# Kernel optimization log

Hardware: AMD Instinct MI355X
Metric: run time of the kernel (lower is better)

Reference implementation:

```python
import jax, jax.numpy as jnp
import numpy as np

N = 100_000      # nodes
E = 1_600_000    # edges (avg degree 16)
C_IN = 32
C_OUT = 32


def setup_inputs() -> dict:
    key = jax.random.key(0)
    ks = jax.random.split(key, 8)
    x = jax.random.normal(ks[0], (N, C_IN), jnp.float32)
    edge_index = jax.random.randint(ks[1], (2, E), 0, N)
    edge_weight = jax.random.uniform(ks[2], (E,), jnp.float32)
    h = jax.random.normal(ks[3], (N, C_OUT), jnp.float32)
    s_in = 1.0 / np.sqrt(C_IN)
    s_out = 1.0 / np.sqrt(C_OUT)
    # 6 ChebConvs (gates z, r, h-tilde; each has an x-conv and an h-conv), K=2
    Wx = jax.random.normal(ks[4], (3, 2, C_IN, C_OUT), jnp.float32) * s_in
    bx = jnp.zeros((3, C_OUT), jnp.float32)
    Wh = jax.random.normal(ks[5], (3, 2, C_OUT, C_OUT), jnp.float32) * s_out
    bh = jnp.zeros((3, C_OUT), jnp.float32)
    Wl = jax.random.normal(ks[6], (C_OUT, 1), jnp.float32) * s_out
    bl = jnp.zeros((1,), jnp.float32)
    return dict(x=x, edge_index=edge_index, edge_weight=edge_weight, h=h,
                Wx=Wx, bx=bx, Wh=Wh, bh=bh, Wl=Wl, bl=bl)


def _cheb(v, W, b, coef, src, dst, n):
    # ChebConv, K=2, sym norm, lambda_max=2:
    #   T0 = v ; T1 = Lhat @ v, Lhat = -D^{-1/2} A D^{-1/2} (zero diagonal)
    t1 = jax.ops.segment_sum(coef[:, None] * v[src], dst, num_segments=n)
    return v @ W[0] + t1 @ W[1] + b


def reference(x, edge_index, edge_weight, h, Wx, bx, Wh, bh, Wl, bl):
    n = x.shape[0]
    src, dst = edge_index[0], edge_index[1]
    deg = jax.ops.segment_sum(edge_weight, src, num_segments=n)
    safe = jnp.where(deg > 0, deg, 1.0)
    dis = jnp.where(deg > 0, jax.lax.rsqrt(safe), 0.0)
    coef = -(dis[src] * edge_weight * dis[dst])  # scaled-Laplacian edge coeffs

    def gate(g, v_x, v_h):
        return (_cheb(v_x, Wx[g], bx[g], coef, src, dst, n)
                + _cheb(v_h, Wh[g], bh[g], coef, src, dst, n))

    z = jax.nn.sigmoid(gate(0, x, h))          # update gate
    r = jax.nn.sigmoid(gate(1, x, h))          # reset gate
    h_tilde = jnp.tanh(gate(2, x, h * r))      # candidate state
    h_new = z * h + (1.0 - z) * h_tilde
    out = jax.nn.softplus(jax.nn.relu(h_new) @ Wl + bl)  # [N, 1]
    return (out, h_new)
```

## Files before the change

kernel.cpp:

```cpp
#include <hip/hip_runtime.h>
#include <math.h>

#define NN 100000
#define NE 1600000
#define C  32
#define CAP 48

#define BSH    8
#define BNODES 256
#define NB     392
#define BCAP   4608
#define EPB    4096

#define WQ_SCALE 32767.0f
#define INV_WQ   (1.0f/32767.0f)
#define DEG_FIX  4194304.0f
#define INV_DEG_FIX (1.0f/4194304.0f)

typedef __attribute__((ext_vector_type(8))) short short8;
typedef __attribute__((ext_vector_type(4))) float floatx4;

__device__ __forceinline__ unsigned rn_bf16(float f) {
    unsigned b = __float_as_uint(f);
    return (b + 0x7fffu + ((b >> 16) & 1u)) >> 16;
}

__device__ __forceinline__ float sigm(float a) { return 1.f / (1.f + expf(-a)); }

__device__ __forceinline__ unsigned enc_edge(int s, float w) {
    int wq = (int)(w * WQ_SCALE + 0.5f);
    wq = wq > 32767 ? 32767 : wq;
    return ((unsigned)s << 15) | (unsigned)wq;
}

__device__ __forceinline__ short8 pack_hi8(uint4 a, uint4 b) {
    short8 v;
    v[0] = (short)(a.x >> 16); v[1] = (short)(a.y >> 16);
    v[2] = (short)(a.z >> 16); v[3] = (short)(a.w >> 16);
    v[4] = (short)(b.x >> 16); v[5] = (short)(b.y >> 16);
    v[6] = (short)(b.z >> 16); v[7] = (short)(b.w >> 16);
    return v;
}
__device__ __forceinline__ short8 pack_lo8(uint4 a, uint4 b) {
    short8 v;
    v[0] = (short)(a.x & 0xffffu); v[1] = (short)(a.y & 0xffffu);
    v[2] = (short)(a.z & 0xffffu); v[3] = (short)(a.w & 0xffffu);
    v[4] = (short)(b.x & 0xffffu); v[5] = (short)(b.y & 0xffffu);
    v[6] = (short)(b.z & 0xffffu); v[7] = (short)(b.w & 0xffffu);
    return v;
}

__global__ __launch_bounds__(256) void bin_pass(const int* __restrict__ ei,
                                                const float* __restrict__ w,
                                                int* __restrict__ gbin_d,
                                                int* __restrict__ gbin_s,
                                                uint2* __restrict__ drec,
                                                unsigned* __restrict__ srec) {
    __shared__ int hd[NB], hs[NB], bd[NB], bs[NB];
    int tid = threadIdx.x;
    for (int i = tid; i < NB; i += 256) { hd[i] = 0; hs[i] = 0; }
    __syncthreads();
    int e0 = blockIdx.x * EPB;
    for (int i = tid; i < EPB; i += 256) {
        int e = e0 + i;
        if (e < NE) {
            atomicAdd(&hs[ei[e] >> BSH], 1);
            atomicAdd(&hd[ei[NE + e] >> BSH], 1);
        }
    }
    __syncthreads();
    for (int i = tid; i < NB; i += 256) {
        bd[i] = hd[i] ? atomicAdd(&gbin_d[i], hd[i]) : 0;
        bs[i] = hs[i] ? atomicAdd(&gbin_s[i], hs[i]) : 0;
    }
    __syncthreads();
    for (int i = tid; i < NB; i += 256) { hd[i] = 0; hs[i] = 0; }
    __syncthreads();
    for (int i = tid; i < EPB; i += 256) {
        int e = e0 + i;
        if (e < NE) {
            int s = ei[e], d = ei[NE + e];
            float we = w[e];
            int dbin = d >> BSH;
            int off = bd[dbin] + atomicAdd(&hd[dbin], 1);
            if (off < BCAP)
                drec[(size_t)dbin * BCAP + off] =
                    make_uint2(((unsigned)s << BSH) | (unsigned)(d & (BNODES - 1)),
                               __float_as_uint(we));
            int sbin = s >> BSH;
            int offs = bs[sbin] + atomicAdd(&hs[sbin], 1);
            if (offs < BCAP)
                srec[(size_t)sbin * BCAP + offs] =
                    ((unsigned)(s & (BNODES - 1)) << 22) | (unsigned)(we * DEG_FIX);
        }
    }
}

__global__ __launch_bounds__(256) void bin_build(const uint2* __restrict__ drec,
                                                 const unsigned* __restrict__ srec,
                                                 const int* __restrict__ gbin_d,
                                                 const int* __restrict__ gbin_s,
                                                 unsigned* __restrict__ buckets,
                                                 int* __restrict__ cursor,
                                                 float* __restrict__ dis) {
    __shared__ __align__(16) unsigned lbuck[BNODES * CAP];
    __shared__ int lcur[BNODES];
    __shared__ int ldeg[BNODES];
    int b = blockIdx.x, tid = threadIdx.x;
    if (tid < BNODES) { lcur[tid] = 0; ldeg[tid] = 0; }
    __syncthreads();
    int cnt_d = min(gbin_d[b], BCAP);
    int cnt_s = min(gbin_s[b], BCAP);
    for (int i = tid; i < cnt_d; i += 256) {
        uint2 r = drec[(size_t)b * BCAP + i];
        int d8 = r.x & (BNODES - 1);
        int s  = (int)(r.x >> BSH);
        int pos = atomicAdd(&lcur[d8], 1);
        if (pos < CAP) lbuck[d8 * CAP + pos] = enc_edge(s, __uint_as_float(r.y));
    }
    for (int i = tid; i < cnt_s; i += 256) {
        unsigned r = srec[(size_t)b * BCAP + i];
        atomicAdd(&ldeg[r >> 22], (int)(r & 0x3FFFFFu));
    }
    __syncthreads();
    uint4* gb = (uint4*)(buckets + (size_t)b * BNODES * CAP);
    const uint4* lb = (const uint4*)lbuck;
    for (int i = tid; i < BNODES * CAP / 4; i += 256) gb[i] = lb[i];
    int n = b * BNODES + tid;
    if (tid < BNODES && n < NN) {
        cursor[n] = lcur[tid];
        int di = ldeg[tid];
        dis[n] = di > 0 ? rsqrtf((float)di * INV_DEG_FIX) : 0.f;
    }
}

__global__ __launch_bounds__(256) void build_xh(const float* __restrict__ x,
                                                const float* __restrict__ h,
                                                const float* __restrict__ dis,
                                                unsigned* __restrict__ xh2,
                                                unsigned* __restrict__ xraw2) {
    int t = blockIdx.x * 256 + threadIdx.x;
    if (t >= NN * C) return;
    float d = dis[t >> 5];
    float xv = x[t], hv = h[t];
    xh2[t]   = (rn_bf16(xv * d) << 16) | rn_bf16(hv * d);
    xraw2[t] = (rn_bf16(xv) << 16) | rn_bf16(hv);
}

__global__ __launch_bounds__(256) void agg_xh(const unsigned* __restrict__ buckets,
                                              const int* __restrict__ cursor,
                                              const float* __restrict__ dis,
                                              const unsigned* __restrict__ xh2,
                                              unsigned* __restrict__ agg2) {
    int tid = threadIdx.x;
    int nl = tid >> 5, j = tid & 31;
    int n = blockIdx.x * 8 + nl;
    if (n >= NN) return;
    int cnt = min(cursor[n], CAP);
    float ax0 = 0.f, ax1 = 0.f, ax2 = 0.f, ax3 = 0.f;
    float ah0 = 0.f, ah1 = 0.f, ah2 = 0.f, ah3 = 0.f;
    for (int base = 0; base < cnt; base += 32) {
        int idx = base + j;
        int sv = 0; float cv = 0.f;
        if (idx < cnt) {
            unsigned u = buckets[(size_t)n * CAP + idx];
            sv = (int)(u >> 15);
            cv = (float)(u & 32767u) * INV_WQ;
        }
        int mm = min(32, cnt - base);
        int i2 = 0;
        for (; i2 + 4 <= mm; i2 += 4) {
            int s0 = __shfl(sv, i2 + 0, 32); float c0 = __shfl(cv, i2 + 0, 32);
            int s1 = __shfl(sv, i2 + 1, 32); float c1 = __shfl(cv, i2 + 1, 32);
            int s2 = __shfl(sv, i2 + 2, 32); float c2 = __shfl(cv, i2 + 2, 32);
            int s3 = __shfl(sv, i2 + 3, 32); float c3 = __shfl(cv, i2 + 3, 32);
            unsigned u0 = xh2[(size_t)s0 * C + j];
            unsigned u1 = xh2[(size_t)s1 * C + j];
            unsigned u2 = xh2[(size_t)s2 * C + j];
            unsigned u3 = xh2[(size_t)s3 * C + j];
            ax0 = fmaf(c0, __uint_as_float(u0 & 0xffff0000u), ax0);
            ah0 = fmaf(c0, __uint_as_float(u0 << 16), ah0);
            ax1 = fmaf(c1, __uint_as_float(u1 & 0xffff0000u), ax1);
            ah1 = fmaf(c1, __uint_as_float(u1 << 16), ah1);
            ax2 = fmaf(c2, __uint_as_float(u2 & 0xffff0000u), ax2);
            ah2 = fmaf(c2, __uint_as_float(u2 << 16), ah2);
            ax3 = fmaf(c3, __uint_as_float(u3 & 0xffff0000u), ax3);
            ah3 = fmaf(c3, __uint_as_float(u3 << 16), ah3);
        }
        for (; i2 < mm; ++i2) {
            int s = __shfl(sv, i2, 32); float cf = __shfl(cv, i2, 32);
            unsigned u = xh2[(size_t)s * C + j];
            ax0 = fmaf(cf, __uint_as_float(u & 0xffff0000u), ax0);
            ah0 = fmaf(cf, __uint_as_float(u << 16), ah0);
        }
    }
    float disn = -dis[n];
    float ax = disn * ((ax0 + ax1) + (ax2 + ax3));
    float ah = disn * ((ah0 + ah1) + (ah2 + ah3));
    agg2[(size_t)n * C + j] = (rn_bf16(ax) << 16) | rn_bf16(ah);
}

__global__ __launch_bounds__(256) void gate_mfma(const unsigned* __restrict__ xraw2,
                                                 const unsigned* __restrict__ agg2,
                                                 const float* __restrict__ dis,
                                                 const float* __restrict__ Wx,
                                                 const float* __restrict__ Wh,
                                                 const float* __restrict__ bx,
                                                 const float* __restrict__ bh,
                                                 unsigned* __restrict__ hrz2,
                                                 unsigned short* __restrict__ hr16,
                                                 float* __restrict__ pout) {
    __shared__ __align__(16) unsigned short Bl[20][64][8];
    int tid = threadIdx.x;
    for (int i = tid; i < 20 * 64; i += 256) {
        int f = i >> 6, l = i & 63;
        int t, c;
        if (f < 16) { t = f >> 2; c = f & 3; }
        else        { t = 4 + ((f - 16) >> 1); c = (f - 16) & 1; }
        int g = t >> 1;
        int j = ((t & 1) << 4) + (l & 15);
        int kb = (l >> 4) << 3;
        const float* srcp = (c < 2 ? Wx : Wh) + g * 2048 + (c & 1) * 1024 + j;
        unsigned pk[4];
#pragma unroll
        for (int q = 0; q < 4; ++q) {
            unsigned lo = rn_bf16(srcp[(kb + 2 * q) * 32]);
            unsigned hi = rn_bf16(srcp[(kb + 2 * q + 1) * 32]);
            pk[q] = (hi << 16) | lo;
        }
        *(uint4*)(&Bl[f][l][0]) = make_uint4(pk[0], pk[1], pk[2], pk[3]);
    }

    int lane = tid & 63, wave = tid >> 6;
    int j0 = lane & 15, quad = lane >> 4;
    int tbase = blockIdx.x * 64 + wave * 16;
    int na = tbase + j0;
    short8 A0 = {0,0,0,0,0,0,0,0}, A1 = A0, A2 = A0, A3 = A0;
    if (na < NN) {
        const uint4* px = (const uint4*)(xraw2 + (size_t)na * C + quad * 8);
        uint4 xa = px[0], xb = px[1];
        A0 = pack_hi8(xa, xb);
        A2 = pack_lo8(xa, xb);
        const uint4* pg = (const uint4*)(agg2 + (size_t)na * C + quad * 8);
        uint4 ga = pg[0], gb = pg[1];
        A1 = pack_hi8(ga, gb);
        A3 = pack_lo8(ga, gb);
    }
    __syncthreads();

#define B8(f) (*(const short8*)(&Bl[f][lane][0]))
    floatx4 az0 = {0.f,0.f,0.f,0.f}, az1 = az0, ar0 = az0, ar1 = az0, ap0 = az0, ap1 = az0;
    az0 = __builtin_amdgcn_mfma_f32_16x16x32_bf16(A0, B8(0),  az0, 0, 0, 0);
    az0 = __builtin_amdgcn_mfma_f32_16x16x32_bf16(A1, B8(1),  az0, 0, 0, 0);
    az0 = __builtin_amdgcn_mfma_f32_16x16x32_bf16(A2, B8(2),  az0, 0, 0, 0);
    az0 = __builtin_amdgcn_mfma_f32_16x16x32_bf16(A3, B8(3),  az0, 0, 0, 0);
    az1 = __builtin_amdgcn_mfma_f32_16x16x32_bf16(A0, B8(4),  az1, 0, 0, 0);
    az1 = __builtin_amdgcn_mfma_f32_16x16x32_bf16(A1, B8(5),  az1, 0, 0, 0);
    az1 = __builtin_amdgcn_mfma_f32_16x16x32_bf16(A2, B8(6),  az1, 0, 0, 0);
    az1 = __builtin_amdgcn_mfma_f32_16x16x32_bf16(A3, B8(7),  az1, 0, 0, 0);
    ar0 = __builtin_amdgcn_mfma_f32_16x16x32_bf16(A0, B8(8),  ar0, 0, 0, 0);
    ar0 = __builtin_amdgcn_mfma_f32_16x16x32_bf16(A1, B8(9),  ar0, 0, 0, 0);
    ar0 = __builtin_amdgcn_mfma_f32_16x16x32_bf16(A2, B8(10), ar0, 0, 0, 0);
    ar0 = __builtin_amdgcn_mfma_f32_16x16x32_bf16(A3, B8(11), ar0, 0, 0, 0);
    ar1 = __builtin_amdgcn_mfma_f32_16x16x32_bf16(A0, B8(12), ar1, 0, 0, 0);
    ar1 = __builtin_amdgcn_mfma_f32_16x16x32_bf16(A1, B8(13), ar1, 0, 0, 0);
    ar1 = __builtin_amdgcn_mfma_f32_16x16x32_bf16(A2, B8(14), ar1, 0, 0, 0);
    ar1 = __builtin_amdgcn_mfma_f32_16x16x32_bf16(A3, B8(15), ar1, 0, 0, 0);
    ap0 = __builtin_amdgcn_mfma_f32_16x16x32_bf16(A0, B8(16), ap0, 0, 0, 0);
    ap0 = __builtin_amdgcn_mfma_f32_16x16x32_bf16(A1, B8(17), ap0, 0, 0, 0);
    ap1 = __builtin_amdgcn_mfma_f32_16x16x32_bf16(A0, B8(18), ap1, 0, 0, 0);
    ap1 = __builtin_amdgcn_mfma_f32_16x16x32_bf16(A1, B8(19), ap1, 0, 0, 0);
#undef B8

    float bza = bx[j0]      + bh[j0];
    float bzb = bx[j0 + 16] + bh[j0 + 16];
    float bra = bx[32 + j0] + bh[32 + j0];
    float brb = bx[48 + j0] + bh[48 + j0];
    float bpa = bx[64 + j0] + bh[64 + j0];
    float bpb = bx[80 + j0] + bh[80 + j0];
#pragma unroll
    for (int p = 0; p < 4; ++p) {
        int nr = tbase + quad * 4 + p;
        if (nr >= NN) continue;
        float dn = dis[nr];
        size_t ra = (size_t)nr * C + j0;
        size_t rb = ra + 16;
        float ha = __uint_as_float(xraw2[ra] << 16);
        float hb = __uint_as_float(xraw2[rb] << 16);
        float za  = sigm(az0[p] + bza);
        float zb  = sigm(az1[p] + bzb);
        float rav = sigm(ar0[p] + bra);
        float rbv = sigm(ar1[p] + brb);
        float hra = ha * rav, hrb = hb * rbv;
        hrz2[ra] = (rn_bf16(hra) << 16) | rn_bf16(za);
        hrz2[rb] = (rn_bf16(hrb) << 16) | rn_bf16(zb);
        hr16[ra] = (unsigned short)rn_bf16(dn * hra);
        hr16[rb] = (unsigned short)rn_bf16(dn * hrb);
        pout[ra] = ap0[p] + bpa;
        pout[rb] = ap1[p] + bpb;
    }
}

__global__ __launch_bounds__(256) void final_kernel(const float* __restrict__ h,
                                                    const unsigned* __restrict__ hrz2,
                                                    const float* __restrict__ ph,
                                                    const unsigned* __restrict__ buckets,
                                                    const int* __restrict__ cursor,
                                                    const float* __restrict__ dis,
                                                    const unsigned short* __restrict__ hr16,
                                                    const float* __restrict__ Wh,
                                                    const float* __restrict__ Wl,
                                                    const float* __restrict__ bl,
                                                    float* __restrict__ out,
                                                    float* __restrict__ hnew) {
    __shared__ float sW[2 * 1024];
    __shared__ float sIn[2][8][C];
    int tid = threadIdx.x;
    for (int i = tid; i < 2 * 1024; i += 256) sW[i] = Wh[4096 + i];
    int nl = tid >> 5, j = tid & 31;
    int n = blockIdx.x * 8 + nl;
    if (n >= NN) return;

    int cnt = min(cursor[n], CAP);
    float a0 = 0.f, a1 = 0.f, a2 = 0.f, a3 = 0.f;
    for (int base = 0; base < cnt; base += 32) {
        int idx = base + j;
        int sv = 0; float cv = 0.f;
        if (idx < cnt) {
            unsigned u = buckets[(size_t)n * CAP + idx];
            sv = (int)(u >> 15);
            cv = (float)(u & 32767u) * INV_WQ;
        }
        int mm = min(32, cnt - base);
        int i2 = 0;
        for (; i2 + 4 <= mm; i2 += 4) {
            int s0 = __shfl(sv, i2 + 0, 32); float c0 = __shfl(cv, i2 + 0, 32);
            int s1 = __shfl(sv, i2 + 1, 32); float c1 = __shfl(cv, i2 + 1, 32);
            int s2 = __shfl(sv, i2 + 2, 32); float c2 = __shfl(cv, i2 + 2, 32);
            int s3 = __shfl(sv, i2 + 3, 32); float c3 = __shfl(cv, i2 + 3, 32);
            float v0 = __uint_as_float(((unsigned)hr16[(size_t)s0 * C + j]) << 16);
            float v1 = __uint_as_float(((unsigned)hr16[(size_t)s1 * C + j]) << 16);
            float v2 = __uint_as_float(((unsigned)hr16[(size_t)s2 * C + j]) << 16);
            float v3 = __uint_as_float(((unsigned)hr16[(size_t)s3 * C + j]) << 16);
            a0 = fmaf(c0, v0, a0);
            a1 = fmaf(c1, v1, a1);
            a2 = fmaf(c2, v2, a2);
            a3 = fmaf(c3, v3, a3);
        }
        for (; i2 < mm; ++i2) {
            int s = __shfl(sv, i2, 32); float cf = __shfl(cv, i2, 32);
            a0 = fmaf(cf, __uint_as_float(((unsigned)hr16[(size_t)s * C + j]) << 16), a0);
        }
    }
    float ag = -dis[n] * ((a0 + a1) + (a2 + a3));
    unsigned uz = hrz2[(size_t)n * C + j];
    float hrv = __uint_as_float(uz & 0xffff0000u);
    float zv  = __uint_as_float(uz << 16);
    sIn[0][nl][j] = hrv;
    sIn[1][nl][j] = ag;
    __syncthreads();

    float acc = ph[(size_t)n * C + j];
#pragma unroll
    for (int k = 0; k < C; ++k) {
        int o = k * 32 + j;
        acc = fmaf(sIn[0][nl][k], sW[o], acc);
        acc = fmaf(sIn[1][nl][k], sW[1024 + o], acc);
    }
    float ht = tanhf(acc);
    float hv = h[(size_t)n * C + j];
    float hn = fmaf(zv, hv - ht, ht);
    hnew[(size_t)n * C + j] = hn;
    float p = fmaxf(hn, 0.f) * Wl[j];
#pragma unroll
    for (int off = 16; off; off >>= 1) p += __shfl_down(p, off, 32);
    if (j == 0) {
        float v = p + bl[0];
        out[n] = fmaxf(v, 0.f) + log1pf(expf(-fabsf(v)));
    }
}

extern "C" void kernel_launch(void* const* d_in, const int* in_sizes, int n_in,
                              void* d_out, int out_size, void* d_ws, size_t ws_size,
                              hipStream_t stream) {
    const float* x  = (const float*)d_in[0];
    const int*   ei = (const int*)d_in[1];
    const float* ew = (const float*)d_in[2];
    const float* h  = (const float*)d_in[3];
    const float* Wx = (const float*)d_in[4];
    const float* bx = (const float*)d_in[5];
    const float* Wh = (const float*)d_in[6];
    const float* bh = (const float*)d_in[7];
    const float* Wl = (const float*)d_in[8];
    const float* bl = (const float*)d_in[9];

    float* out  = (float*)d_out;
    float* hnew = out + NN;

    char* ws = (char*)d_ws;
    int*            gbin_d = (int*)ws;
    int*            gbin_s = gbin_d + NB;
    uint2*          drec   = (uint2*)(ws + 4096);
    unsigned*       srec   = (unsigned*)(drec + (size_t)NB * BCAP);
    unsigned*       buckets= srec + (size_t)NB * BCAP;
    int*            cursor = (int*)(buckets + (size_t)NB * BNODES * CAP);
    float*          dis    = (float*)(cursor + NN);
    unsigned*       xh2    = (unsigned*)(dis + NN);
    unsigned*       agg2   = xh2 + (size_t)NN * C;
    float*          pbuf   = (float*)(agg2 + (size_t)NN * C);
    unsigned*       xraw2  = (unsigned*)drec;
    unsigned short* hr16   = (unsigned short*)srec;
    unsigned*       hrz2   = xh2;

    hipMemsetAsync(d_ws, 0, 4096, stream);

    bin_pass    <<<(NE + EPB - 1) / EPB, 256, 0, stream>>>(ei, ew, gbin_d, gbin_s,
                                                           drec, srec);
    bin_build   <<<NB, 256, 0, stream>>>(drec, srec, gbin_d, gbin_s,
                                         buckets, cursor, dis);
    build_xh    <<<(NN * C + 255) / 256, 256, 0, stream>>>(x, h, dis, xh2, xraw2);
    agg_xh      <<<(NN + 7) / 8, 256, 0, stream>>>(buckets, cursor, dis, xh2, agg2);
    gate_mfma   <<<(NN + 63) / 64, 256, 0, stream>>>(xraw2, agg2, dis, Wx, Wh,
                                                     bx, bh, hrz2, hr16, pbuf);
    final_kernel<<<(NN + 7) / 8, 256, 0, stream>>>(h, hrz2, pbuf,
                                                   buckets, cursor, dis, hr16,
                                                   Wh, Wl, bl, out, hnew);
}
```

Measured before the change: 289.9 us.

## Replace two-pass binned edge bucketing with direct global-atomic scatter

Replaces the two-kernel binning pipeline (shared-memory histogram, per-bin staging records, then per-bin local bucket build) with a single edge_scatter kernel. It uses global float atomics for degree and a global int atomic cursor per destination node to write encoded edges straight into per-node buckets. The degree rsqrt moves into build_xh. This removes one launch and the staging round-trip through global memory, at the cost of about 3.2M scattered global atomics. Bucket order and float degree sums now depend on atomic ordering, so results are no longer deterministic.

Result: slower. 381.5 us (+31.6%).

```diff
diff --git a/kernel.cpp b/kernel.cpp
--- a/kernel.cpp
+++ b/kernel.cpp
@@ -6,16 +6,8 @@
 #define C  32
 #define CAP 48
 
-#define BSH    8
-#define BNODES 256
-#define NB     392
-#define BCAP   4608
-#define EPB    4096
-
 #define WQ_SCALE 32767.0f
 #define INV_WQ   (1.0f/32767.0f)
-#define DEG_FIX  4194304.0f
-#define INV_DEG_FIX (1.0f/4194304.0f)
 
 typedef __attribute__((ext_vector_type(8))) short short8;
 typedef __attribute__((ext_vector_type(4))) float floatx4;
@@ -50,98 +42,39 @@
     return v;
 }
 
-__global__ __launch_bounds__(256) void bin_pass(const int* __restrict__ ei,
-                                                const float* __restrict__ w,
-                                                int* __restrict__ gbin_d,
-                                                int* __restrict__ gbin_s,
-                                                uint2* __restrict__ drec,
-                                                unsigned* __restrict__ srec) {
-    __shared__ int hd[NB], hs[NB], bd[NB], bs[NB];
-    int tid = threadIdx.x;
-    for (int i = tid; i < NB; i += 256) { hd[i] = 0; hs[i] = 0; }
-    __syncthreads();
-    int e0 = blockIdx.x * EPB;
-    for (int i = tid; i < EPB; i += 256) {
-        int e = e0 + i;
-        if (e < NE) {
-            atomicAdd(&hs[ei[e] >> BSH], 1);
-            atomicAdd(&hd[ei[NE + e] >> BSH], 1);
-        }
-    }
-    __syncthreads();
-    for (int i = tid; i < NB; i += 256) {
-        bd[i] = hd[i] ? atomicAdd(&gbin_d[i], hd[i]) : 0;
-        bs[i] = hs[i] ? atomicAdd(&gbin_s[i], hs[i]) : 0;
-    }
-    __syncthreads();
-    for (int i = tid; i < NB; i += 256) { hd[i] = 0; hs[i] = 0; }
-    __syncthreads();
-    for (int i = tid; i < EPB; i += 256) {
-        int e = e0 + i;
-        if (e < NE) {
-            int s = ei[e], d = ei[NE + e];
-            float we = w[e];
-            int dbin = d >> BSH;
-            int off = bd[dbin] + atomicAdd(&hd[dbin], 1);
-            if (off < BCAP)
-                drec[(size_t)dbin * BCAP + off] =
-                    make_uint2(((unsigned)s << BSH) | (unsigned)(d & (BNODES - 1)),
-                               __float_as_uint(we));
-            int sbin = s >> BSH;
-            int offs = bs[sbin] + atomicAdd(&hs[sbin], 1);
-            if (offs < BCAP)
-                srec[(size_t)sbin * BCAP + offs] =
-                    ((unsigned)(s & (BNODES - 1)) << 22) | (unsigned)(we * DEG_FIX);
-        }
-    }
-}
-
-__global__ __launch_bounds__(256) void bin_build(const uint2* __restrict__ drec,
-                                                 const unsigned* __restrict__ srec,
-                                                 const int* __restrict__ gbin_d,
-                                                 const int* __restrict__ gbin_s,
-                                                 unsigned* __restrict__ buckets,
-                                                 int* __restrict__ cursor,
-                                                 float* __restrict__ dis) {
-    __shared__ __align__(16) unsigned lbuck[BNODES * CAP];
-    __shared__ int lcur[BNODES];
-    __shared__ int ldeg[BNODES];
-    int b = blockIdx.x, tid = threadIdx.x;
-    if (tid < BNODES) { lcur[tid] = 0; ldeg[tid] = 0; }
-    __syncthreads();
-    int cnt_d = min(gbin_d[b], BCAP);
-    int cnt_s = min(gbin_s[b], BCAP);
-    for (int i = tid; i < cnt_d; i += 256) {
-        uint2 r = drec[(size_t)b * BCAP + i];
-        int d8 = r.x & (BNODES - 1);
-        int s  = (int)(r.x >> BSH);
-        int pos = atomicAdd(&lcur[d8], 1);
-        if (pos < CAP) lbuck[d8 * CAP + pos] = enc_edge(s, __uint_as_float(r.y));
-    }
-    for (int i = tid; i < cnt_s; i += 256) {
-        unsigned r = srec[(size_t)b * BCAP + i];
-        atomicAdd(&ldeg[r >> 22], (int)(r & 0x3FFFFFu));
-    }
-    __syncthreads();
-    uint4* gb = (uint4*)(buckets + (size_t)b * BNODES * CAP);
-    const uint4* lb = (const uint4*)lbuck;
-    for (int i = tid; i < BNODES * CAP / 4; i += 256) gb[i] = lb[i];
-    int n = b * BNODES + tid;
-    if (tid < BNODES && n < NN) {
-        cursor[n] = lcur[tid];
-        int di = ldeg[tid];
-        dis[n] = di > 0 ? rsqrtf((float)di * INV_DEG_FIX) : 0.f;
+__global__ __launch_bounds__(256) void edge_scatter(const int* __restrict__ ei,
+                                                    const float* __restrict__ w,
+                                                    float* __restrict__ deg,
+                                                    int* __restrict__ cursor,
+                                                    unsigned* __restrict__ buckets) {
+    int e0 = (blockIdx.x * 256 + threadIdx.x) * 4;
+    if (e0 >= NE) return;
+    int4   s4 = *(const int4*)(ei + e0);
+    int4   d4 = *(const int4*)(ei + NE + e0);
+    float4 w4 = *(const float4*)(w + e0);
+    int   ss[4] = {s4.x, s4.y, s4.z, s4.w};
+    int   dd[4] = {d4.x, d4.y, d4.z, d4.w};
+    float ww[4] = {w4.x, w4.y, w4.z, w4.w};
+#pragma unroll
+    for (int i = 0; i < 4; ++i) {
+        atomicAdd(&deg[ss[i]], ww[i]);
+        int pos = atomicAdd(&cursor[dd[i]], 1);
+        if (pos < CAP)
+            buckets[(size_t)dd[i] * CAP + pos] = enc_edge(ss[i], ww[i]);
     }
 }
 
 __global__ __launch_bounds__(256) void build_xh(const float* __restrict__ x,
                                                 const float* __restrict__ h,
-                                                const float* __restrict__ dis,
+                                                const float* __restrict__ deg,
+                                                float* __restrict__ dis,
                                                 unsigned* __restrict__ xh2,
                                                 unsigned* __restrict__ xraw2) {
     int t = blockIdx.x * 256 + threadIdx.x;
     if (t >= NN * C) return;
-    float d = dis[t >> 5];
+    float dg = deg[t >> 5];
+    float d = dg > 0.f ? rsqrtf(dg) : 0.f;
+    if ((t & 31) == 0) dis[t >> 5] = d;
     float xv = x[t], hv = h[t];
     xh2[t]   = (rn_bf16(xv * d) << 16) | rn_bf16(hv * d);
     xraw2[t] = (rn_bf16(xv) << 16) | rn_bf16(hv);
@@ -398,27 +331,23 @@
     float* hnew = out + NN;
 
     char* ws = (char*)d_ws;
-    int*            gbin_d = (int*)ws;
-    int*            gbin_s = gbin_d + NB;
-    uint2*          drec   = (uint2*)(ws + 4096);
-    unsigned*       srec   = (unsigned*)(drec + (size_t)NB * BCAP);
-    unsigned*       buckets= srec + (size_t)NB * BCAP;
-    int*            cursor = (int*)(buckets + (size_t)NB * BNODES * CAP);
+    float*          deg    = (float*)ws;
+    int*            cursor = (int*)(deg + NN);
     float*          dis    = (float*)(cursor + NN);
-    unsigned*       xh2    = (unsigned*)(dis + NN);
-    unsigned*       agg2   = xh2 + (size_t)NN * C;
+    unsigned*       buckets= (unsigned*)(dis + NN);
+    unsigned*       xh2    = buckets + (size_t)NN * CAP;
+    unsigned*       xraw2  = xh2 + (size_t)NN * C;
+    unsigned*       agg2   = xraw2 + (size_t)NN * C;
     float*          pbuf   = (float*)(agg2 + (size_t)NN * C);
-    unsigned*       xraw2  = (unsigned*)drec;
-    unsigned short* hr16   = (unsigned short*)srec;
+    unsigned short* hr16   = (unsigned short*)(pbuf + (size_t)NN * C);
     unsigned*       hrz2   = xh2;
 
-    hipMemsetAsync(d_ws, 0, 4096, stream);
-
-    bin_pass    <<<(NE + EPB - 1) / EPB, 256, 0, stream>>>(ei, ew, gbin_d, gbin_s,
-                                                           drec, srec);
-    bin_build   <<<NB, 256, 0, stream>>>(drec, srec, gbin_d, gbin_s,
-                                         buckets, cursor, dis);
-    build_xh    <<<(NN * C + 255) / 256, 256, 0, stream>>>(x, h, dis, xh2, xraw2);
+    hipMemsetAsync(d_ws, 0, (size_t)NN * 8, stream);
+
+    edge_scatter<<<(NE / 4 + 255) / 256, 256, 0, stream>>>(ei, ew, deg, cursor,
+                                                           buckets);
+    build_xh    <<<(NN * C + 255) / 256, 256, 0, stream>>>(x, h, deg, dis,
+                                                           xh2, xraw2);
     agg_xh      <<<(NN + 7) / 8, 256, 0, stream>>>(buckets, cursor, dis, xh2, agg2);
     gate_mfma   <<<(NN + 63) / 64, 256, 0, stream>>>(xraw2, agg2, dis, Wx, Wh,
                                                      bx, bh, hrz2, hr16, pbuf);
```
